# Performance work log

Measured on AMD Instinct MI355X. Metric: run time of the kernel, lower is better.

The kernel has to match this reference:

```python
import jax, jax.numpy as jnp
import numpy as np

N_EMBD = 768
N_HEAD = 12
HEAD_DIM = N_EMBD // N_HEAD
B = 4
L_MAIN = 1024
L_SIDE = 1024
HALF = L_SIDE // 2  # occurrences of each modality per row
LN_EPS = 1e-5


def setup_inputs() -> dict:
    key = jax.random.key(0)
    ks = jax.random.split(key, 16)
    x = jax.random.normal(ks[0], (B, L_MAIN, N_EMBD), jnp.float32)
    # ages in years, sorted per-row (events arrive in time order), all >= 0
    age = jnp.sort(jax.random.uniform(ks[1], (B, L_MAIN), jnp.float32) * 80.0, axis=1)
    mod_age = jnp.sort(jax.random.uniform(ks[2], (B, L_SIDE), jnp.float32) * 80.0, axis=1)
    # each row holds exactly HALF tokens of modality 2 and HALF of modality 3, randomly interleaved
    base = jnp.concatenate([jnp.full((HALF,), 2, jnp.int32), jnp.full((HALF,), 3, jnp.int32)])
    mod_idx = jax.vmap(lambda k: jax.random.permutation(k, base))(jax.random.split(ks[3], B))
    mod2_emb = jax.random.normal(ks[4], (B * HALF, N_EMBD), jnp.float32)
    mod3_emb = jax.random.normal(ks[5], (B * HALF, N_EMBD), jnp.float32)

    def lin(k, fan_out, fan_in):
        return 0.02 * jax.random.normal(k, (fan_out, fan_in), jnp.float32)

    params = dict(
        ln0_w=jnp.ones((N_EMBD,), jnp.float32), ln0_b=jnp.zeros((N_EMBD,), jnp.float32),
        ln1_w=jnp.ones((N_EMBD,), jnp.float32), ln1_b=jnp.zeros((N_EMBD,), jnp.float32),
        ln2_w=jnp.ones((N_EMBD,), jnp.float32), ln2_b=jnp.zeros((N_EMBD,), jnp.float32),
        q_w=lin(ks[6], N_EMBD, N_EMBD), q_b=jnp.zeros((N_EMBD,), jnp.float32),
        k_w=lin(ks[7], N_EMBD, N_EMBD), k_b=jnp.zeros((N_EMBD,), jnp.float32),
        v_w=lin(ks[8], N_EMBD, N_EMBD), v_b=jnp.zeros((N_EMBD,), jnp.float32),
        c_w=lin(ks[9], N_EMBD, N_EMBD), c_b=jnp.zeros((N_EMBD,), jnp.float32),
        fc_w=lin(ks[10], 4 * N_EMBD, N_EMBD), fc_b=jnp.zeros((4 * N_EMBD,), jnp.float32),
        proj_w=lin(ks[11], N_EMBD, 4 * N_EMBD), proj_b=jnp.zeros((N_EMBD,), jnp.float32),
    )
    return dict(x=x, age=age, mod_idx=mod_idx, mod_age=mod_age,
                mod2_emb=mod2_emb, mod3_emb=mod3_emb, **params)


def _ln(t, w, b):
    m = jnp.mean(t, axis=-1, keepdims=True)
    v = jnp.var(t, axis=-1, keepdims=True)
    return (t - m) * jax.lax.rsqrt(v + LN_EPS) * w + b


def _fuse_embed(mod_idx, mod_age, mod2_emb, mod3_emb):
    # torch: stable argsort by age, then scatter each modality's embeddings into
    # its matching positions in row-major nonzero order.
    order = jnp.argsort(mod_age, axis=1, stable=True)
    s_idx = jnp.take_along_axis(mod_idx, order, axis=1)  # [B, L_side]
    rows = jnp.arange(s_idx.shape[0])[:, None]
    def scatter_mod(val, m_emb):
        mask = s_idx == val
        occ = jnp.cumsum(mask, axis=1) - 1          # per-row occurrence counter
        gidx = rows * HALF + jnp.clip(occ, 0, HALF - 1)  # global row-major index
        return jnp.where(mask[..., None], m_emb[gidx], 0.0)
    return scatter_mod(2, mod2_emb) + scatter_mod(3, mod3_emb)


def _cross_fusion(x, age, mod_idx, mod_age, mod2_emb, mod3_emb,
                  ln0_w, ln0_b, ln1_w, ln1_b, ln2_w, ln2_b,
                  q_w, q_b, k_w, k_b, v_w, v_b, c_w, c_b,
                  fc_w, fc_b, proj_w, proj_b):
    mod_x = _fuse_embed(mod_idx, mod_age, mod2_emb, mod3_emb)  # [B, L_side, E]
    # time_attention_mask: query may attend to keys with key_age <= query_age, pad = key_age >= 0
    attn_mask = (age[:, :, None] >= mod_age[:, None, :]) & (mod_age >= 0.0)[:, None, :]
    attn_mask = attn_mask[:, None, :, :]  # [B, 1, L_main, L_side]

    xn = _ln(x, ln1_w, ln1_b)
    sn = _ln(mod_x, ln0_w, ln0_b)
    q = (xn @ q_w.T + q_b).reshape(B, L_MAIN, N_HEAD, HEAD_DIM).transpose(0, 2, 1, 3)
    k = (sn @ k_w.T + k_b).reshape(B, L_SIDE, N_HEAD, HEAD_DIM).transpose(0, 2, 1, 3)
    v = (sn @ v_w.T + v_b).reshape(B, L_SIDE, N_HEAD, HEAD_DIM).transpose(0, 2, 1, 3)

    att = jnp.einsum('bhqd,bhkd->bhqk', q, k) * (HEAD_DIM ** -0.5)
    all_masked = ~jnp.any(attn_mask, axis=-1, keepdims=True)
    # fully-masked rows: use 0 logits (uniform softmax) then zero out -> matches
    # torch's masked_fill(all_masked, 0) after nan softmax, but grad-safe.
    neg = jnp.where(all_masked, 0.0, -jnp.inf)
    att = jnp.where(attn_mask, att, neg)
    att = jax.nn.softmax(att, axis=-1)
    att = jnp.where(all_masked, 0.0, att)

    y = jnp.einsum('bhqk,bhkd->bhqd', att, v)
    y = y.transpose(0, 2, 1, 3).reshape(B, L_MAIN, N_EMBD)
    x = x + (y @ c_w.T + c_b)
    h = _ln(x, ln2_w, ln2_b)
    h = jax.nn.gelu(h @ fc_w.T + fc_b, approximate=False)
    x = x + (h @ proj_w.T + proj_b)
    return x


def reference(x, age, mod_idx, mod_age, mod2_emb, mod3_emb,
              ln0_w, ln0_b, ln1_w, ln1_b, ln2_w, ln2_b,
              q_w, q_b, k_w, k_b, v_w, v_b, c_w, c_b,
              fc_w, fc_b, proj_w, proj_b):
    return _cross_fusion(x, age, mod_idx, mod_age, mod2_emb, mod3_emb,
                         ln0_w, ln0_b, ln1_w, ln1_b, ln2_w, ln2_b,
                         q_w, q_b, k_w, k_b, v_w, v_b, c_w, c_b,
                         fc_w, fc_b, proj_w, proj_b)
```

## Files before the change

kernel.cpp:

```cpp
#include <hip/hip_runtime.h>

#define N_EMBD 768
#define SEQ    1024
#define NBATCH 4
#define NHEAD  12
#define HDIM   64
#define NROWS  4096
#define FFN    3072
#define W768   589824
#define WFC    2359296

typedef unsigned short u16;
typedef __bf16 bf16x8 __attribute__((ext_vector_type(8)));
typedef float  f32x4  __attribute__((ext_vector_type(4)));
typedef unsigned short u16x8 __attribute__((ext_vector_type(8)));

typedef const __attribute__((address_space(1))) unsigned int gu32;
typedef __attribute__((address_space(3))) unsigned int lu32;
#define GLL(g, l) __builtin_amdgcn_global_load_lds((gu32*)(g), (lu32*)(l), 16, 0, 0)

__device__ __forceinline__ u16 f2bf(float f) {
    union { float f; unsigned int i; } v; v.f = f;
    unsigned int r = v.i + 0x7fffu + ((v.i >> 16) & 1u);
    return (u16)(r >> 16);
}

__global__ __launch_bounds__(256) void cvt_weights(const float* __restrict__ qw,
                                                   const float* __restrict__ kw,
                                                   const float* __restrict__ vw,
                                                   const float* __restrict__ cw,
                                                   const float* __restrict__ fcw,
                                                   const float* __restrict__ pw,
                                                   u16* __restrict__ dst) {
    size_t e = ((size_t)blockIdx.x * 256 + threadIdx.x) * 4;
    const float* src; size_t base;
    if      (e < 1 * (size_t)W768) { src = qw;  base = 0; }
    else if (e < 2 * (size_t)W768) { src = kw;  base = 1 * (size_t)W768; }
    else if (e < 3 * (size_t)W768) { src = vw;  base = 2 * (size_t)W768; }
    else if (e < 4 * (size_t)W768) { src = cw;  base = 3 * (size_t)W768; }
    else if (e < 4 * (size_t)W768 + WFC) { src = fcw; base = 4 * (size_t)W768; }
    else { src = pw; base = 4 * (size_t)W768 + WFC; }
    float4 v = *(const float4*)(src + (e - base));
    ushort4 o;
    o.x = f2bf(v.x); o.y = f2bf(v.y); o.z = f2bf(v.z); o.w = f2bf(v.w);
    *(ushort4*)(dst + e) = o;
}

__global__ __launch_bounds__(1024) void prefix_kernel(const int* __restrict__ mod_idx,
                                                      int* __restrict__ g) {
    __shared__ int sc[1024];
    int b = blockIdx.x, j = threadIdx.x;
    int mi  = mod_idx[b * SEQ + j];
    int is2 = (mi == 2) ? 1 : 0;
    sc[j] = is2;
    __syncthreads();
    for (int off = 1; off < 1024; off <<= 1) {
        int add = (j >= off) ? sc[j - off] : 0;
        __syncthreads();
        sc[j] += add;
        __syncthreads();
    }
    int c2  = sc[j];
    int occ = is2 ? (c2 - 1) : (j - c2);
    occ = occ < 0 ? 0 : (occ > 511 ? 511 : occ);
    g[b * SEQ + j] = is2 ? (b * 512 + occ) : (2048 + b * 512 + occ);
}

__global__ __launch_bounds__(256) void ln_rows(const float* __restrict__ src,
                                               const float* __restrict__ src2,
                                               const int* __restrict__ g,
                                               const float* __restrict__ w,
                                               const float* __restrict__ b,
                                               u16* __restrict__ dst) {
    int row  = blockIdx.x * 4 + (threadIdx.x >> 6);
    int lane = threadIdx.x & 63;
    const float* p;
    if (g) {
        int gi = g[row];
        p = (gi < 2048) ? (src + (size_t)gi * N_EMBD)
                        : (src2 + (size_t)(gi - 2048) * N_EMBD);
    } else {
        p = src + (size_t)row * N_EMBD;
    }
    float vals[12];
    float s = 0.f, sq = 0.f;
#pragma unroll
    for (int c = 0; c < 12; c++) {
        float v = p[c * 64 + lane];
        vals[c] = v; s += v; sq += v * v;
    }
#pragma unroll
    for (int o = 32; o > 0; o >>= 1) { s += __shfl_xor(s, o); sq += __shfl_xor(sq, o); }
    float mean = s * (1.0f / 768.0f);
    float var  = sq * (1.0f / 768.0f) - mean * mean;
    float r    = rsqrtf(var + 1e-5f);
    u16* d = dst + (size_t)row * N_EMBD;
#pragma unroll
    for (int c = 0; c < 12; c++) {
        int idx = c * 64 + lane;
        d[idx] = f2bf((vals[c] - mean) * r * w[idx] + b[idx]);
    }
}

__device__ __forceinline__ void core128(const u16* __restrict__ A, const u16* __restrict__ W,
                                        int K, int m0, int n0, int t,
                                        u16* As, u16* Bs, f32x4 (&acc)[4][4]) {
    int w = t >> 6, lane = t & 63, quad = lane >> 4, l16 = lane & 15;
    int r16 = lane >> 2, c8 = (lane & 3) * 8;
    int wm = (w >> 1) * 64, wn = (w & 1) * 64;
    for (int k0 = 0; k0 < K; k0 += 32) {
        __syncthreads();
        const u16* ga = A + (size_t)(m0 + w * 32 + r16) * K + k0 + c8;
        const u16* gb = W + (size_t)(n0 + w * 32 + r16) * K + k0 + c8;
        GLL(ga,                  &As[(w * 32) * 32]);
        GLL(ga + 16 * (size_t)K, &As[(w * 32 + 16) * 32]);
        GLL(gb,                  &Bs[(w * 32) * 32]);
        GLL(gb + 16 * (size_t)K, &Bs[(w * 32 + 16) * 32]);
        __syncthreads();
        bf16x8 af[4], bfr[4];
#pragma unroll
        for (int i = 0; i < 4; i++)
            af[i] = *(const bf16x8*)&As[(wm + i * 16 + l16) * 32 + quad * 8];
#pragma unroll
        for (int j = 0; j < 4; j++)
            bfr[j] = *(const bf16x8*)&Bs[(wn + j * 16 + l16) * 32 + quad * 8];
#pragma unroll
        for (int i = 0; i < 4; i++)
#pragma unroll
            for (int j = 0; j < 4; j++)
                acc[i][j] = __builtin_amdgcn_mfma_f32_16x16x32_bf16(af[i], bfr[j], acc[i][j], 0, 0, 0);
    }
}

__device__ __forceinline__ void core64(const u16* __restrict__ A, const u16* __restrict__ W,
                                       int K, int kBeg, int kEnd, int m0, int n0, int t,
                                       u16* As, u16* Bs, f32x4 (&acc)[2][4]) {
    int w = t >> 6, lane = t & 63, quad = lane >> 4, l16 = lane & 15;
    int r16 = lane >> 2, c8 = (lane & 3) * 8;
    int wm = (w >> 1) * 32, wn = (w & 1) * 64;
    for (int k0 = kBeg; k0 < kEnd; k0 += 32) {
        __syncthreads();
        const u16* gb = W + (size_t)(n0 + w * 32 + r16) * K + k0 + c8;
        GLL(A + (size_t)(m0 + w * 16 + r16) * K + k0 + c8, &As[(w * 16) * 32]);
        GLL(gb,                  &Bs[(w * 32) * 32]);
        GLL(gb + 16 * (size_t)K, &Bs[(w * 32 + 16) * 32]);
        __syncthreads();
        bf16x8 af[2], bfr[4];
#pragma unroll
        for (int i = 0; i < 2; i++)
            af[i] = *(const bf16x8*)&As[(wm + i * 16 + l16) * 32 + quad * 8];
#pragma unroll
        for (int j = 0; j < 4; j++)
            bfr[j] = *(const bf16x8*)&Bs[(wn + j * 16 + l16) * 32 + quad * 8];
#pragma unroll
        for (int i = 0; i < 2; i++)
#pragma unroll
            for (int j = 0; j < 4; j++)
                acc[i][j] = __builtin_amdgcn_mfma_f32_16x16x32_bf16(af[i], bfr[j], acc[i][j], 0, 0, 0);
    }
}

__global__ __launch_bounds__(256) void gemm_qkv(const u16* __restrict__ xn,
                                                const u16* __restrict__ sn,
                                                const u16* __restrict__ wq,
                                                const float* __restrict__ qb,
                                                const float* __restrict__ kb,
                                                const float* __restrict__ vb,
                                                u16* __restrict__ outbase) {
    __shared__ u16 As[128 * 32], Bs[128 * 32];
    int z = blockIdx.z;
    const u16* A = (z == 0) ? xn : sn;
    const u16* W = wq + (size_t)z * W768;
    const float* bias = (z == 0) ? qb : ((z == 1) ? kb : vb);
    u16* C = outbase + (size_t)z * ((size_t)NROWS * N_EMBD);
    int m0 = blockIdx.y * 128, n0 = blockIdx.x * 128;
    int t = threadIdx.x;
    f32x4 acc[4][4];
#pragma unroll
    for (int i = 0; i < 4; i++)
#pragma unroll
        for (int j = 0; j < 4; j++) acc[i][j] = (f32x4){0.f, 0.f, 0.f, 0.f};
    core128(A, W, N_EMBD, m0, n0, t, As, Bs, acc);
    int w = t >> 6, lane = t & 63, quad = lane >> 4, l16 = lane & 15;
    int wm = (w >> 1) * 64, wn = (w & 1) * 64;
#pragma unroll
    for (int j = 0; j < 4; j++) {
        int col = n0 + wn + j * 16 + l16;
        float bv = bias[col];
#pragma unroll
        for (int i = 0; i < 4; i++) {
            int rowb = m0 + wm + i * 16 + quad * 4;
#pragma unroll
            for (int r = 0; r < 4; r++)
                C[(size_t)(rowb + r) * N_EMBD + col] = f2bf(acc[i][j][r] + bv);
        }
    }
}

__global__ __launch_bounds__(256) void gemm_fc(const u16* __restrict__ A,
                                               const u16* __restrict__ W,
                                               const float* __restrict__ bias,
                                               u16* __restrict__ C) {
    __shared__ u16 As[128 * 32], Bs[128 * 32];
    int m0 = blockIdx.y * 128, n0 = blockIdx.x * 128;
    int t = threadIdx.x;
    f32x4 acc[4][4];
#pragma unroll
    for (int i = 0; i < 4; i++)
#pragma unroll
        for (int j = 0; j < 4; j++) acc[i][j] = (f32x4){0.f, 0.f, 0.f, 0.f};
    core128(A, W, N_EMBD, m0, n0, t, As, Bs, acc);
    int w = t >> 6, lane = t & 63, quad = lane >> 4, l16 = lane & 15;
    int wm = (w >> 1) * 64, wn = (w & 1) * 64;
#pragma unroll
    for (int j = 0; j < 4; j++) {
        int col = n0 + wn + j * 16 + l16;
        float bv = bias[col];
#pragma unroll
        for (int i = 0; i < 4; i++) {
            int rowb = m0 + wm + i * 16 + quad * 4;
#pragma unroll
            for (int r = 0; r < 4; r++) {
                float v = acc[i][j][r] + bv;
                v = 0.5f * v * (1.0f + erff(v * 0.70710678118654752f));
                C[(size_t)(rowb + r) * FFN + col] = f2bf(v);
            }
        }
    }
}

__global__ __launch_bounds__(256) void gemm_cproj(const u16* __restrict__ A,
                                                  const u16* __restrict__ W,
                                                  const float* __restrict__ bias,
                                                  const float* __restrict__ Res,
                                                  float* __restrict__ C) {
    __shared__ u16 As[64 * 32], Bs[128 * 32];
    int m0 = blockIdx.y * 64, n0 = blockIdx.x * 128;
    int t = threadIdx.x;
    f32x4 acc[2][4];
#pragma unroll
    for (int i = 0; i < 2; i++)
#pragma unroll
        for (int j = 0; j < 4; j++) acc[i][j] = (f32x4){0.f, 0.f, 0.f, 0.f};
    core64(A, W, N_EMBD, 0, N_EMBD, m0, n0, t, As, Bs, acc);
    int w = t >> 6, lane = t & 63, quad = lane >> 4, l16 = lane & 15;
    int wm = (w >> 1) * 32, wn = (w & 1) * 64;
#pragma unroll
    for (int j = 0; j < 4; j++) {
        int col = n0 + wn + j * 16 + l16;
        float bv = bias[col];
#pragma unroll
        for (int i = 0; i < 2; i++) {
            int rowb = m0 + wm + i * 16 + quad * 4;
#pragma unroll
            for (int r = 0; r < 4; r++) {
                size_t idx = (size_t)(rowb + r) * N_EMBD + col;
                C[idx] = acc[i][j][r] + bv + Res[idx];
            }
        }
    }
}

__global__ __launch_bounds__(256) void gemm_proj_split(const u16* __restrict__ A,
                                                       const u16* __restrict__ W,
                                                       float* __restrict__ p0,
                                                       float* __restrict__ p1) {
    __shared__ u16 As[64 * 32], Bs[128 * 32];
    int z = blockIdx.z;
    float* P = z ? p1 : p0;
    int m0 = blockIdx.y * 64, n0 = blockIdx.x * 128;
    int t = threadIdx.x;
    f32x4 acc[2][4];
#pragma unroll
    for (int i = 0; i < 2; i++)
#pragma unroll
        for (int j = 0; j < 4; j++) acc[i][j] = (f32x4){0.f, 0.f, 0.f, 0.f};
    core64(A, W, FFN, z * (FFN / 2), (z + 1) * (FFN / 2), m0, n0, t, As, Bs, acc);
    int w = t >> 6, lane = t & 63, quad = lane >> 4, l16 = lane & 15;
    int wm = (w >> 1) * 32, wn = (w & 1) * 64;
#pragma unroll
    for (int j = 0; j < 4; j++) {
        int col = n0 + wn + j * 16 + l16;
#pragma unroll
        for (int i = 0; i < 2; i++) {
            int rowb = m0 + wm + i * 16 + quad * 4;
#pragma unroll
            for (int r = 0; r < 4; r++)
                P[(size_t)(rowb + r) * N_EMBD + col] = acc[i][j][r];
        }
    }
}

__global__ __launch_bounds__(256) void reduce_proj(const float* __restrict__ p0,
                                                   const float* __restrict__ p1,
                                                   const float* __restrict__ bias,
                                                   const float* __restrict__ x1,
                                                   float* __restrict__ out) {
    size_t idx = ((size_t)blockIdx.x * 256 + threadIdx.x) * 4;
    int col = (int)(idx % N_EMBD);
    float4 a = *(const float4*)(p0 + idx);
    float4 b = *(const float4*)(p1 + idx);
    float4 r = *(const float4*)(x1 + idx);
    float4 bb = *(const float4*)(bias + col);
    float4 o;
    o.x = a.x + b.x + r.x + bb.x;
    o.y = a.y + b.y + r.y + bb.y;
    o.z = a.z + b.z + r.z + bb.z;
    o.w = a.w + b.w + r.w + bb.w;
    *(float4*)(out + idx) = o;
}

#define KST 72

__global__ __launch_bounds__(256) void attn_kernel(const u16* __restrict__ Q,
                                                   const u16* __restrict__ K,
                                                   const u16* __restrict__ V,
                                                   const float* __restrict__ age,
                                                   const float* __restrict__ mod_age,
                                                   u16* __restrict__ Y) {
    __shared__ u16 Kl[64 * KST];
    __shared__ u16 Vt[64 * KST];
    __shared__ u16 Pl[4][16 * KST];

    int bx = blockIdx.x;
    int qt = 15 - (bx / 48);
    int bh = bx % 48;
    int b = bh / NHEAD, h = bh % NHEAD;
    int t = threadIdx.x;
    int w = t >> 6, lane = t & 63, quad = lane >> 4, l16 = lane & 15;
    int q0 = qt * 64 + w * 16;

    size_t qrowbase = ((size_t)(b * SEQ + q0 + l16)) * N_EMBD + h * HDIM;
    bf16x8 qf0 = *(const bf16x8*)&Q[qrowbase + quad * 8];
    bf16x8 qf1 = *(const bf16x8*)&Q[qrowbase + 32 + quad * 8];

    float age_r[4];
#pragma unroll
    for (int r = 0; r < 4; r++) age_r[r] = age[b * SEQ + q0 + quad * 4 + r];
    float age_q0      = __shfl(age_r[0], 0);
    float age_max_blk = age[b * SEQ + qt * 64 + 63];
    float mod_min     = mod_age[b * SEQ];

    float mv0 = (lane < 16) ? mod_age[b * SEQ + lane * 64] : 1e30f;
    unsigned long long bm = __ballot(mv0 > age_max_blk);
    int nkt = bm ? (__ffsll(bm) - 1) : 16;

    int krow0 = t >> 3,        kc8 = (t & 7) * 8;
    int krow1 = 32 + (t >> 3);
    int vrow  = t & 63;
    int vc8_0 = t >> 6, vc8_1 = 4 + (t >> 6);

    float m_i[4] = {-1e30f, -1e30f, -1e30f, -1e30f};
    float l_i[4] = {0.f, 0.f, 0.f, 0.f};
    f32x4 o[4];
#pragma unroll
    for (int nt = 0; nt < 4; nt++) o[nt] = (f32x4){0.f, 0.f, 0.f, 0.f};

    u16x8 kr0, kr1, vr0, vr1;
    float mreg = 0.f;
    if (nkt > 0) {
        size_t kb = ((size_t)(b * SEQ)) * N_EMBD + h * HDIM;
        kr0 = *(const u16x8*)(K + kb + (size_t)krow0 * N_EMBD + kc8);
        kr1 = *(const u16x8*)(K + kb + (size_t)krow1 * N_EMBD + kc8);
        vr0 = *(const u16x8*)(V + kb + (size_t)vrow * N_EMBD + vc8_0 * 8);
        vr1 = *(const u16x8*)(V + kb + (size_t)vrow * N_EMBD + vc8_1 * 8);
        mreg = mod_age[b * SEQ + lane];
    }

    for (int kt = 0; kt < nkt; kt++) {
        __syncthreads();
        *(u16x8*)&Kl[krow0 * KST + kc8] = kr0;
        *(u16x8*)&Kl[krow1 * KST + kc8] = kr1;
#pragma unroll
        for (int e = 0; e < 8; e++) Vt[(vc8_0 * 8 + e) * KST + vrow] = vr0[e];
#pragma unroll
        for (int e = 0; e < 8; e++) Vt[(vc8_1 * 8 + e) * KST + vrow] = vr1[e];
        float mcur = mreg;
        __syncthreads();

        if (kt + 1 < nkt) {
            size_t kb = ((size_t)(b * SEQ + (kt + 1) * 64)) * N_EMBD + h * HDIM;
            kr0 = *(const u16x8*)(K + kb + (size_t)krow0 * N_EMBD + kc8);
            kr1 = *(const u16x8*)(K + kb + (size_t)krow1 * N_EMBD + kc8);
            vr0 = *(const u16x8*)(V + kb + (size_t)vrow * N_EMBD + vc8_0 * 8);
            vr1 = *(const u16x8*)(V + kb + (size_t)vrow * N_EMBD + vc8_1 * 8);
            mreg = mod_age[b * SEQ + (kt + 1) * 64 + lane];
        }

        float tile_max = __shfl(mcur, 63);
        bool need_mask = tile_max > age_q0;
        float p[4][4];
#pragma unroll
        for (int jt = 0; jt < 4; jt++) {
            f32x4 s = (f32x4){0.f, 0.f, 0.f, 0.f};
            bf16x8 kf0 = *(const bf16x8*)&Kl[(jt * 16 + l16) * KST + quad * 8];
            bf16x8 kf1 = *(const bf16x8*)&Kl[(jt * 16 + l16) * KST + 32 + quad * 8];
            s = __builtin_amdgcn_mfma_f32_16x16x32_bf16(qf0, kf0, s, 0, 0, 0);
            s = __builtin_amdgcn_mfma_f32_16x16x32_bf16(qf1, kf1, s, 0, 0, 0);
            float mval = __shfl(mcur, jt * 16 + l16);
#pragma unroll
            for (int r = 0; r < 4; r++) {
                float sv = s[r] * 0.125f;
                p[jt][r] = (!need_mask || mval <= age_r[r]) ? sv : -1e30f;
            }
        }
        float alpha[4];
#pragma unroll
        for (int r = 0; r < 4; r++) {
            float mx = fmaxf(fmaxf(p[0][r], p[1][r]), fmaxf(p[2][r], p[3][r]));
#pragma unroll
            for (int msk = 1; msk < 16; msk <<= 1) mx = fmaxf(mx, __shfl_xor(mx, msk));
            float mnew = fmaxf(m_i[r], mx);
            alpha[r] = __expf(m_i[r] - mnew);
            float srow = 0.f;
#pragma unroll
            for (int jt = 0; jt < 4; jt++) {
                float pv = __expf(p[jt][r] - mnew);
                p[jt][r] = pv;
                srow += pv;
            }
#pragma unroll
            for (int msk = 1; msk < 16; msk <<= 1) srow += __shfl_xor(srow, msk);
            l_i[r] = l_i[r] * alpha[r] + srow;
            m_i[r] = mnew;
        }
#pragma unroll
        for (int jt = 0; jt < 4; jt++)
#pragma unroll
            for (int r = 0; r < 4; r++)
                Pl[w][(quad * 4 + r) * KST + jt * 16 + l16] = f2bf(p[jt][r]);
#pragma unroll
        for (int nt = 0; nt < 4; nt++)
#pragma unroll
            for (int r = 0; r < 4; r++) o[nt][r] *= alpha[r];
#pragma unroll
        for (int c = 0; c < 2; c++) {
            bf16x8 pf = *(const bf16x8*)&Pl[w][l16 * KST + c * 32 + quad * 8];
#pragma unroll
            for (int nt = 0; nt < 4; nt++) {
                bf16x8 vf = *(const bf16x8*)&Vt[(nt * 16 + l16) * KST + c * 32 + quad * 8];
                o[nt] = __builtin_amdgcn_mfma_f32_16x16x32_bf16(pf, vf, o[nt], 0, 0, 0);
            }
        }
    }
#pragma unroll
    for (int r = 0; r < 4; r++) {
        int qrow = q0 + quad * 4 + r;
        float inv = (age_r[r] >= mod_min) ? (1.0f / l_i[r]) : 0.0f;
#pragma unroll
        for (int nt = 0; nt < 4; nt++)
            Y[((size_t)(b * SEQ + qrow)) * N_EMBD + h * HDIM + nt * 16 + l16] =
                f2bf(o[nt][r] * inv);
    }
}

extern "C" void kernel_launch(void* const* d_in, const int* in_sizes, int n_in,
                              void* d_out, int out_size, void* d_ws, size_t ws_size,
                              hipStream_t stream) {
    const float* x       = (const float*)d_in[0];
    const float* age     = (const float*)d_in[1];
    const int*   mod_idx = (const int*)d_in[2];
    const float* mod_age = (const float*)d_in[3];
    const float* mod2    = (const float*)d_in[4];
    const float* mod3    = (const float*)d_in[5];
    const float* ln0w = (const float*)d_in[6],  *ln0b = (const float*)d_in[7];
    const float* ln1w = (const float*)d_in[8],  *ln1b = (const float*)d_in[9];
    const float* ln2w = (const float*)d_in[10], *ln2b = (const float*)d_in[11];
    const float* qb = (const float*)d_in[13];
    const float* kb = (const float*)d_in[15];
    const float* vb = (const float*)d_in[17];
    const float* cb = (const float*)d_in[19];
    const float* fcb = (const float*)d_in[21];
    const float* pb = (const float*)d_in[23];

    char* ws = (char*)d_ws;
    const size_t RB = (size_t)NROWS * N_EMBD * 2;
    int* g   = (int*)ws;
    u16* wq  = (u16*)(ws + 32768);
    u16* wc  = wq + 3 * (size_t)W768;
    u16* wfc = wq + 4 * (size_t)W768;
    u16* wp  = wq + 4 * (size_t)W768 + WFC;
    size_t off = 32768 + 2 * (4 * (size_t)W768 + 2 * (size_t)WFC);
    u16* xn   = (u16*)(ws + off); off += RB;
    u16* sn   = (u16*)(ws + off); off += RB;
    u16* qbuf = (u16*)(ws + off); off += RB;
    u16* kbuf = (u16*)(ws + off); off += RB;
    u16* vbuf = (u16*)(ws + off); off += RB;
    float* x1 = (float*)(ws + off); off += (size_t)NROWS * N_EMBD * 4;
    u16* hbuf = (u16*)(ws + off);
    u16* yb = xn;  u16* hn = qbuf;
    float* p0 = (float*)xn;
    float* p1 = (float*)kbuf;

    cvt_weights<<<(4 * W768 + 2 * WFC) / 1024, 256, 0, stream>>>(
        (const float*)d_in[12], (const float*)d_in[14], (const float*)d_in[16],
        (const float*)d_in[18], (const float*)d_in[20], (const float*)d_in[22], wq);
    prefix_kernel<<<NBATCH, 1024, 0, stream>>>(mod_idx, g);
    ln_rows<<<NROWS / 4, 256, 0, stream>>>(x, nullptr, nullptr, ln1w, ln1b, xn);
    ln_rows<<<NROWS / 4, 256, 0, stream>>>(mod2, mod3, g, ln0w, ln0b, sn);

    gemm_qkv<<<dim3(N_EMBD / 128, NROWS / 128, 3), 256, 0, stream>>>(xn, sn, wq, qb, kb, vb, qbuf);

    attn_kernel<<<NBATCH * NHEAD * 16, 256, 0, stream>>>(qbuf, kbuf, vbuf, age, mod_age, yb);

    gemm_cproj<<<dim3(N_EMBD / 128, NROWS / 64), 256, 0, stream>>>(yb, wc, cb, x, x1);
    ln_rows<<<NROWS / 4, 256, 0, stream>>>(x1, nullptr, nullptr, ln2w, ln2b, hn);
    gemm_fc<<<dim3(FFN / 128, NROWS / 128), 256, 0, stream>>>(hn, wfc, fcb, hbuf);
    gemm_proj_split<<<dim3(N_EMBD / 128, NROWS / 64, 2), 256, 0, stream>>>(hbuf, wp, p0, p1);
    reduce_proj<<<(NROWS * N_EMBD / 4) / 256, 256, 0, stream>>>(p0, p1, pb, x1, (float*)d_out);

    (void)in_sizes; (void)n_in; (void)out_size; (void)ws_size;
}
```

Measured before the change: 314.1 us.

## Fuse prep kernels, double GEMM k-step to 64, use tanh-form GELU

Merges the weight conversion, the first LayerNorm and the modality prefix scan into a single launch to cut kernel-launch overhead. The prefix scan now uses 256 threads with 4 elements each. All GEMM cores load a 64-wide K slab per barrier pair instead of 32, which halves the number of synchronisations but doubles shared memory per block. The exact erf GELU is replaced by a sigmoid-based tanh approximation, which may add error against the reference.

```diff
diff --git a/kernel.cpp b/kernel.cpp
--- a/kernel.cpp
+++ b/kernel.cpp
@@ -9,6 +9,7 @@
 #define FFN    3072
 #define W768   589824
 #define WFC    2359296
+#define NCVT   6912
 
 typedef unsigned short u16;
 typedef __bf16 bf16x8 __attribute__((ext_vector_type(8)));
@@ -25,45 +26,81 @@
     return (u16)(r >> 16);
 }
 
-__global__ __launch_bounds__(256) void cvt_weights(const float* __restrict__ qw,
+__global__ __launch_bounds__(256) void prep_kernel(const float* __restrict__ qw,
                                                    const float* __restrict__ kw,
                                                    const float* __restrict__ vw,
                                                    const float* __restrict__ cw,
                                                    const float* __restrict__ fcw,
                                                    const float* __restrict__ pw,
-                                                   u16* __restrict__ dst) {
-    size_t e = ((size_t)blockIdx.x * 256 + threadIdx.x) * 4;
-    const float* src; size_t base;
-    if      (e < 1 * (size_t)W768) { src = qw;  base = 0; }
-    else if (e < 2 * (size_t)W768) { src = kw;  base = 1 * (size_t)W768; }
-    else if (e < 3 * (size_t)W768) { src = vw;  base = 2 * (size_t)W768; }
-    else if (e < 4 * (size_t)W768) { src = cw;  base = 3 * (size_t)W768; }
-    else if (e < 4 * (size_t)W768 + WFC) { src = fcw; base = 4 * (size_t)W768; }
-    else { src = pw; base = 4 * (size_t)W768 + WFC; }
-    float4 v = *(const float4*)(src + (e - base));
-    ushort4 o;
-    o.x = f2bf(v.x); o.y = f2bf(v.y); o.z = f2bf(v.z); o.w = f2bf(v.w);
-    *(ushort4*)(dst + e) = o;
-}
-
-__global__ __launch_bounds__(1024) void prefix_kernel(const int* __restrict__ mod_idx,
-                                                      int* __restrict__ g) {
-    __shared__ int sc[1024];
-    int b = blockIdx.x, j = threadIdx.x;
-    int mi  = mod_idx[b * SEQ + j];
-    int is2 = (mi == 2) ? 1 : 0;
-    sc[j] = is2;
-    __syncthreads();
-    for (int off = 1; off < 1024; off <<= 1) {
-        int add = (j >= off) ? sc[j - off] : 0;
-        __syncthreads();
-        sc[j] += add;
-        __syncthreads();
-    }
-    int c2  = sc[j];
-    int occ = is2 ? (c2 - 1) : (j - c2);
-    occ = occ < 0 ? 0 : (occ > 511 ? 511 : occ);
-    g[b * SEQ + j] = is2 ? (b * 512 + occ) : (2048 + b * 512 + occ);
+                                                   u16* __restrict__ wdst,
+                                                   const float* __restrict__ x,
+                                                   const float* __restrict__ ln1w,
+                                                   const float* __restrict__ ln1b,
+                                                   u16* __restrict__ xn,
+                                                   const int* __restrict__ mod_idx,
+                                                   int* __restrict__ g) {
+    int bx = blockIdx.x;
+    if (bx < NCVT) {
+        size_t e = ((size_t)bx * 256 + threadIdx.x) * 4;
+        const float* src; size_t base;
+        if      (e < 1 * (size_t)W768) { src = qw;  base = 0; }
+        else if (e < 2 * (size_t)W768) { src = kw;  base = 1 * (size_t)W768; }
+        else if (e < 3 * (size_t)W768) { src = vw;  base = 2 * (size_t)W768; }
+        else if (e < 4 * (size_t)W768) { src = cw;  base = 3 * (size_t)W768; }
+        else if (e < 4 * (size_t)W768 + WFC) { src = fcw; base = 4 * (size_t)W768; }
+        else { src = pw; base = 4 * (size_t)W768 + WFC; }
+        float4 v = *(const float4*)(src + (e - base));
+        ushort4 o;
+        o.x = f2bf(v.x); o.y = f2bf(v.y); o.z = f2bf(v.z); o.w = f2bf(v.w);
+        *(ushort4*)(wdst + e) = o;
+    } else if (bx < NCVT + 1024) {
+        int row  = (bx - NCVT) * 4 + (threadIdx.x >> 6);
+        int lane = threadIdx.x & 63;
+        const float* p = x + (size_t)row * N_EMBD;
+        float vals[12];
+        float s = 0.f, sq = 0.f;
+#pragma unroll
+        for (int c = 0; c < 12; c++) {
+            float v = p[c * 64 + lane];
+            vals[c] = v; s += v; sq += v * v;
+        }
+#pragma unroll
+        for (int o = 32; o > 0; o >>= 1) { s += __shfl_xor(s, o); sq += __shfl_xor(sq, o); }
+        float mean = s * (1.0f / 768.0f);
+        float var  = sq * (1.0f / 768.0f) - mean * mean;
+        float r    = rsqrtf(var + 1e-5f);
+        u16* d = xn + (size_t)row * N_EMBD;
+#pragma unroll
+        for (int c = 0; c < 12; c++) {
+            int idx = c * 64 + lane;
+            d[idx] = f2bf((vals[c] - mean) * r * ln1w[idx] + ln1b[idx]);
+        }
+    } else {
+        __shared__ int sc[256];
+        int b = bx - NCVT - 1024;
+        int j = threadIdx.x;
+        int4 mi = *(const int4*)(mod_idx + b * SEQ + j * 4);
+        int f0 = (mi.x == 2), f1 = (mi.y == 2), f2v = (mi.z == 2), f3 = (mi.w == 2);
+        int t1 = f0 + f1, t2 = t1 + f2v, t3 = t2 + f3;
+        sc[j] = t3;
+        __syncthreads();
+        for (int off = 1; off < 256; off <<= 1) {
+            int add = (j >= off) ? sc[j - off] : 0;
+            __syncthreads();
+            sc[j] += add;
+            __syncthreads();
+        }
+        int excl = sc[j] - t3;
+        int cin[4] = {excl + f0, excl + t1, excl + t2, excl + t3};
+        int fl[4] = {f0, f1, f2v, f3};
+#pragma unroll
+        for (int i2 = 0; i2 < 4; i2++) {
+            int jj = j * 4 + i2;
+            int occ = fl[i2] ? (cin[i2] - 1) : (jj - cin[i2]);
+            occ = occ < 0 ? 0 : (occ > 511 ? 511 : occ);
+            g[b * SEQ + jj] = fl[i2] ? (b * 512 + occ) : (2048 + b * 512 + occ);
+        }
+    }
 }
 
 __global__ __launch_bounds__(256) void ln_rows(const float* __restrict__ src,
@@ -108,27 +145,33 @@
     int w = t >> 6, lane = t & 63, quad = lane >> 4, l16 = lane & 15;
     int r16 = lane >> 2, c8 = (lane & 3) * 8;
     int wm = (w >> 1) * 64, wn = (w & 1) * 64;
-    for (int k0 = 0; k0 < K; k0 += 32) {
-        __syncthreads();
-        const u16* ga = A + (size_t)(m0 + w * 32 + r16) * K + k0 + c8;
-        const u16* gb = W + (size_t)(n0 + w * 32 + r16) * K + k0 + c8;
-        GLL(ga,                  &As[(w * 32) * 32]);
-        GLL(ga + 16 * (size_t)K, &As[(w * 32 + 16) * 32]);
-        GLL(gb,                  &Bs[(w * 32) * 32]);
-        GLL(gb + 16 * (size_t)K, &Bs[(w * 32 + 16) * 32]);
-        __syncthreads();
-        bf16x8 af[4], bfr[4];
-#pragma unroll
-        for (int i = 0; i < 4; i++)
-            af[i] = *(const bf16x8*)&As[(wm + i * 16 + l16) * 32 + quad * 8];
-#pragma unroll
-        for (int j = 0; j < 4; j++)
-            bfr[j] = *(const bf16x8*)&Bs[(wn + j * 16 + l16) * 32 + quad * 8];
-#pragma unroll
-        for (int i = 0; i < 4; i++)
+    for (int k0 = 0; k0 < K; k0 += 64) {
+        __syncthreads();
+#pragma unroll
+        for (int hh = 0; hh < 2; hh++) {
+            const u16* ga = A + (size_t)(m0 + w * 32 + r16) * K + k0 + hh * 32 + c8;
+            const u16* gb = W + (size_t)(n0 + w * 32 + r16) * K + k0 + hh * 32 + c8;
+            GLL(ga,                  &As[hh * 4096 + (w * 32) * 32]);
+            GLL(ga + 16 * (size_t)K, &As[hh * 4096 + (w * 32 + 16) * 32]);
+            GLL(gb,                  &Bs[hh * 4096 + (w * 32) * 32]);
+            GLL(gb + 16 * (size_t)K, &Bs[hh * 4096 + (w * 32 + 16) * 32]);
+        }
+        __syncthreads();
+#pragma unroll
+        for (int hh = 0; hh < 2; hh++) {
+            bf16x8 af[4], bfr[4];
+#pragma unroll
+            for (int i = 0; i < 4; i++)
+                af[i] = *(const bf16x8*)&As[hh * 4096 + (wm + i * 16 + l16) * 32 + quad * 8];
 #pragma unroll
             for (int j = 0; j < 4; j++)
-                acc[i][j] = __builtin_amdgcn_mfma_f32_16x16x32_bf16(af[i], bfr[j], acc[i][j], 0, 0, 0);
+                bfr[j] = *(const bf16x8*)&Bs[hh * 4096 + (wn + j * 16 + l16) * 32 + quad * 8];
+#pragma unroll
+            for (int i = 0; i < 4; i++)
+#pragma unroll
+                for (int j = 0; j < 4; j++)
+                    acc[i][j] = __builtin_amdgcn_mfma_f32_16x16x32_bf16(af[i], bfr[j], acc[i][j], 0, 0, 0);
+        }
     }
 }
 
@@ -138,25 +181,31 @@
     int w = t >> 6, lane = t & 63, quad = lane >> 4, l16 = lane & 15;
     int r16 = lane >> 2, c8 = (lane & 3) * 8;
     int wm = (w >> 1) * 32, wn = (w & 1) * 64;
-    for (int k0 = kBeg; k0 < kEnd; k0 += 32) {
-        __syncthreads();
-        const u16* gb = W + (size_t)(n0 + w * 32 + r16) * K + k0 + c8;
-        GLL(A + (size_t)(m0 + w * 16 + r16) * K + k0 + c8, &As[(w * 16) * 32]);
-        GLL(gb,                  &Bs[(w * 32) * 32]);
-        GLL(gb + 16 * (size_t)K, &Bs[(w * 32 + 16) * 32]);
-        __syncthreads();
-        bf16x8 af[2], bfr[4];
-#pragma unroll
-        for (int i = 0; i < 2; i++)
-            af[i] = *(const bf16x8*)&As[(wm + i * 16 + l16) * 32 + quad * 8];
-#pragma unroll
-        for (int j = 0; j < 4; j++)
-            bfr[j] = *(const bf16x8*)&Bs[(wn + j * 16 + l16) * 32 + quad * 8];
-#pragma unroll
-        for (int i = 0; i < 2; i++)
+    for (int k0 = kBeg; k0 < kEnd; k0 += 64) {
+        __syncthreads();
+#pragma unroll
+        for (int hh = 0; hh < 2; hh++) {
+            const u16* gb = W + (size_t)(n0 + w * 32 + r16) * K + k0 + hh * 32 + c8;
+            GLL(A + (size_t)(m0 + w * 16 + r16) * K + k0 + hh * 32 + c8, &As[hh * 2048 + (w * 16) * 32]);
+            GLL(gb,                  &Bs[hh * 4096 + (w * 32) * 32]);
+            GLL(gb + 16 * (size_t)K, &Bs[hh * 4096 + (w * 32 + 16) * 32]);
+        }
+        __syncthreads();
+#pragma unroll
+        for (int hh = 0; hh < 2; hh++) {
+            bf16x8 af[2], bfr[4];
+#pragma unroll
+            for (int i = 0; i < 2; i++)
+                af[i] = *(const bf16x8*)&As[hh * 2048 + (wm + i * 16 + l16) * 32 + quad * 8];
 #pragma unroll
             for (int j = 0; j < 4; j++)
-                acc[i][j] = __builtin_amdgcn_mfma_f32_16x16x32_bf16(af[i], bfr[j], acc[i][j], 0, 0, 0);
+                bfr[j] = *(const bf16x8*)&Bs[hh * 4096 + (wn + j * 16 + l16) * 32 + quad * 8];
+#pragma unroll
+            for (int i = 0; i < 2; i++)
+#pragma unroll
+                for (int j = 0; j < 4; j++)
+                    acc[i][j] = __builtin_amdgcn_mfma_f32_16x16x32_bf16(af[i], bfr[j], acc[i][j], 0, 0, 0);
+        }
     }
 }
 
@@ -167,7 +216,7 @@
                                                 const float* __restrict__ kb,
                                                 const float* __restrict__ vb,
                                                 u16* __restrict__ outbase) {
-    __shared__ u16 As[128 * 32], Bs[128 * 32];
+    __shared__ u16 As[2 * 128 * 32], Bs[2 * 128 * 32];
     int z = blockIdx.z;
     const u16* A = (z == 0) ? xn : sn;
     const u16* W = wq + (size_t)z * W768;
@@ -201,7 +250,7 @@
                                                const u16* __restrict__ W,
                                                const float* __restrict__ bias,
                                                u16* __restrict__ C) {
-    __shared__ u16 As[128 * 32], Bs[128 * 32];
+    __shared__ u16 As[2 * 128 * 32], Bs[2 * 128 * 32];
     int m0 = blockIdx.y * 128, n0 = blockIdx.x * 128;
     int t = threadIdx.x;
     f32x4 acc[4][4];
@@ -222,8 +271,9 @@
 #pragma unroll
             for (int r = 0; r < 4; r++) {
                 float v = acc[i][j][r] + bv;
-                v = 0.5f * v * (1.0f + erff(v * 0.70710678118654752f));
-                C[(size_t)(rowb + r) * FFN + col] = f2bf(v);
+                float y = v * (1.595769122f + 0.071354816f * v * v);
+                float gel = v / (1.0f + __expf(-y));
+                C[(size_t)(rowb + r) * FFN + col] = f2bf(gel);
             }
         }
     }
@@ -234,7 +284,7 @@
                                                   const float* __restrict__ bias,
                                                   const float* __restrict__ Res,
                                                   float* __restrict__ C) {
-    __shared__ u16 As[64 * 32], Bs[128 * 32];
+    __shared__ u16 As[2 * 64 * 32], Bs[2 * 128 * 32];
     int m0 = blockIdx.y * 64, n0 = blockIdx.x * 128;
     int t = threadIdx.x;
     f32x4 acc[2][4];
@@ -265,7 +315,7 @@
                                                        const u16* __restrict__ W,
                                                        float* __restrict__ p0,
                                                        float* __restrict__ p1) {
-    __shared__ u16 As[64 * 32], Bs[128 * 32];
+    __shared__ u16 As[2 * 64 * 32], Bs[2 * 128 * 32];
     int z = blockIdx.z;
     float* P = z ? p1 : p0;
     int m0 = blockIdx.y * 64, n0 = blockIdx.x * 128;
@@ -492,11 +542,10 @@
     float* p0 = (float*)xn;
     float* p1 = (float*)kbuf;
 
-    cvt_weights<<<(4 * W768 + 2 * WFC) / 1024, 256, 0, stream>>>(
+    prep_kernel<<<NCVT + 1024 + NBATCH, 256, 0, stream>>>(
         (const float*)d_in[12], (const float*)d_in[14], (const float*)d_in[16],
-        (const float*)d_in[18], (const float*)d_in[20], (const float*)d_in[22], wq);
-    prefix_kernel<<<NBATCH, 1024, 0, stream>>>(mod_idx, g);
-    ln_rows<<<NROWS / 4, 256, 0, stream>>>(x, nullptr, nullptr, ln1w, ln1b, xn);
+        (const float*)d_in[18], (const float*)d_in[20], (const float*)d_in[22], wq,
+        x, ln1w, ln1b, xn, mod_idx, g);
     ln_rows<<<NROWS / 4, 256, 0, stream>>>(mod2, mod3, g, ln0w, ln0b, sn);
 
     gemm_qkv<<<dim3(N_EMBD / 128, NROWS / 128, 3), 256, 0, stream>>>(xn, sn, wq, qb, kb, vb, qbuf);
```

Result: no change. 313.1 us (-0.3%).
